# Kernel tuning notes

Measured on AMD Instinct MI355X. Metric: run time of the kernel, lower is better.

Reference implementation:

```python
import jax, jax.numpy as jnp
import numpy as np

EPS = 1e-5  # BatchNorm1d default eps
DIMS = [(784, 1024), (1024, 1024), (1024, 1024), (1024, 10)]


def setup_inputs() -> dict:
    key = jax.random.key(0)
    ks = jax.random.split(key, 25)
    d = {"x": jax.random.normal(ks[0], (32768, 784), jnp.float32)}
    for i, (fi, fo) in enumerate(DIMS):
        j = i + 1
        base = 1 + 6 * i
        d[f"W{j}"] = jax.random.uniform(ks[base], (fo, fi), jnp.float32, -1.0, 1.0)
        d[f"b{j}"] = jnp.full((fo,), 0.01, jnp.float32)
        d[f"gamma{j}"] = jax.random.uniform(ks[base + 1], (fo,), jnp.float32, 0.5, 1.5)
        d[f"beta{j}"] = 0.1 * jax.random.normal(ks[base + 2], (fo,), jnp.float32)
        d[f"mean{j}"] = 0.1 * jax.random.normal(ks[base + 3], (fo,), jnp.float32)
        d[f"var{j}"] = jax.random.uniform(ks[base + 4], (fo,), jnp.float32, 0.5, 1.5)
    return d


def _bn(h, gamma, beta, mean, var):
    # inference-mode BatchNorm1d with running stats
    return gamma * (h - mean) * jax.lax.rsqrt(var + EPS) + beta


def reference(x,
              W1, b1, gamma1, beta1, mean1, var1,
              W2, b2, gamma2, beta2, mean2, var2,
              W3, b3, gamma3, beta3, mean3, var3,
              W4, b4, gamma4, beta4, mean4, var4):
    h = x.reshape(-1, 784)
    # layer 1: Quantizer(1) -> BinarizeLinear -> BN -> Hardtanh
    h = jnp.sign(h)
    h = h @ jnp.sign(W1).T + b1
    h = jnp.clip(_bn(h, gamma1, beta1, mean1, var1), -1.0, 1.0)
    # layer 2
    h = jnp.sign(h)
    h = h @ jnp.sign(W2).T + b2
    h = jnp.clip(_bn(h, gamma2, beta2, mean2, var2), -1.0, 1.0)
    # layer 3
    h = jnp.sign(h)
    h = h @ jnp.sign(W3).T + b3
    h = jnp.clip(_bn(h, gamma3, beta3, mean3, var3), -1.0, 1.0)
    # layer 4: Quantizer -> BinarizeLinear -> BN (no hardtanh)
    h = jnp.sign(h)
    h = h @ jnp.sign(W4).T + b4
    return _bn(h, gamma4, beta4, mean4, var4)
```

## Files before the change

kernel.cpp:

```cpp
#include <hip/hip_runtime.h>
#include <cstdint>
#include <climits>


typedef __attribute__((ext_vector_type(4))) int i32x4_t;

__device__ __forceinline__ void gload_lds16(const void* g, void* l) {
  __builtin_amdgcn_global_load_lds(
      (const __attribute__((address_space(1))) unsigned int*)g,
      (__attribute__((address_space(3))) unsigned int*)l, 16, 0, 0);
}

__device__ __forceinline__ int pack4(const float4 v) {
  int b0 = v.x > 0.f ? 1 : (v.x < 0.f ? -1 : 0);
  int b1 = v.y > 0.f ? 1 : (v.y < 0.f ? -1 : 0);
  int b2 = v.z > 0.f ? 1 : (v.z < 0.f ? -1 : 0);
  int b3 = v.w > 0.f ? 1 : (v.w < 0.f ? -1 : 0);
  return (b0 & 0xff) | ((b1 & 0xff) << 8) | ((b2 & 0xff) << 16) | (b3 << 24);
}


__global__ __launch_bounds__(256) void prep_mega_kernel(
    const float* __restrict__ x, int8_t* __restrict__ A0,
    const float* __restrict__ W1f, const float* __restrict__ W2f,
    const float* __restrict__ W3f, const float* __restrict__ W4f,
    int8_t* __restrict__ Wp1, int8_t* __restrict__ Wp2,
    int8_t* __restrict__ Wp3, int8_t* __restrict__ Wp4,
    const float* b1, const float* g1, const float* be1, const float* m1, const float* v1,
    const float* b2, const float* g2, const float* be2, const float* m2, const float* v2,
    const float* b3, const float* g3, const float* be3, const float* m3, const float* v3,
    const float* b4, const float* g4, const float* be4, const float* m4, const float* v4,
    int* __restrict__ T1, int* __restrict__ T2, int* __restrict__ T3,
    int8_t* __restrict__ S1, int8_t* __restrict__ S2, int8_t* __restrict__ S3,
    float* __restrict__ sc4, float* __restrict__ of4) {
  const int b = blockIdx.x;
  const int t = threadIdx.x;
  if (b < 32768) {
    const int col = t * 4;
    if (col < 784) {
      int packed = pack4(*(const float4*)(x + (size_t)b * 784 + col));
      *(int*)(A0 + (size_t)b * 832 + col) = packed;
    } else if (col < 832) {
      *(int*)(A0 + (size_t)b * 832 + col) = 0;
    }
  } else if (b < 35968) {
    const int b2i = b - 32768;
    const float* Wf; int8_t* Wp; int N, K, n, ost;
    if (b2i < 1024)      { Wf = W1f; Wp = Wp1; N = 1024; K = 784;  n = b2i;        ost = 832;  }
    else if (b2i < 2048) { Wf = W2f; Wp = Wp2; N = 1024; K = 1024; n = b2i - 1024; ost = 1024; }
    else if (b2i < 3072) { Wf = W3f; Wp = Wp3; N = 1024; K = 1024; n = b2i - 2048; ost = 1024; }
    else                 { Wf = W4f; Wp = Wp4; N = 10;   K = 1024; n = b2i - 3072; ost = 1024; }
    const int col = t * 4;
    if (col < ost) {
      int packed = 0;
      if (n < N && col + 3 < K)
        packed = pack4(*(const float4*)(Wf + (size_t)n * K + col));
      *(int*)(Wp + (size_t)n * ost + col) = packed;
    }
  } else {
    const int pb = b - 35968;
    if (pb < 12) {
      const int layer = pb >> 2;
      const int n = (pb & 3) * 256 + t;
      const float *bb, *gg, *be, *me, *va; int* T; int8_t* S;
      if (layer == 0)      { bb = b1; gg = g1; be = be1; me = m1; va = v1; T = T1; S = S1; }
      else if (layer == 1) { bb = b2; gg = g2; be = be2; me = m2; va = v2; T = T2; S = S2; }
      else                 { bb = b3; gg = g3; be = be3; me = m3; va = v3; T = T3; S = S3; }
      double g = (double)gg[n];
      double rs = 1.0 / sqrt((double)va[n] + 1e-5);
      int th; int8_t s;
      if (g > 0.0) {
        double tv = (double)me[n] - (double)bb[n] - (double)be[n] / (g * rs);
        tv = fmin(fmax(tv, -2.0e9), 2.0e9);
        th = (int)floor(tv) + 1; s = 1;
      } else if (g < 0.0) {
        double tv = (double)me[n] - (double)bb[n] - (double)be[n] / (g * rs);
        tv = fmin(fmax(tv, -2.0e9), 2.0e9);
        th = (int)ceil(tv); s = -1;
      } else {
        th = INT_MIN; s = (be[n] > 0.f) ? (int8_t)1 : (int8_t)-1;
      }
      T[n] = th; S[n] = s;
    } else if (t < 10) {
      double rs = 1.0 / sqrt((double)v4[t] + 1e-5);
      double sd = (double)g4[t] * rs;
      sc4[t] = (float)sd;
      of4[t] = (float)(sd * ((double)b4[t] - (double)m4[t]) + (double)be4[t]);
    }
  }
}

__global__ __launch_bounds__(512) void gemm_bnn256_kernel(
    const int8_t* __restrict__ A, const int8_t* __restrict__ W,
    int ldk, int nkt,
    const int* __restrict__ T, const int8_t* __restrict__ S,
    int8_t* __restrict__ Aout) {
  __shared__ i32x4_t smem[4096];
  int8_t* sm = (int8_t*)smem;
  const int tid = threadIdx.x;
  const int lane = tid & 63;
  const int w = tid >> 6;
  const int wm = w >> 2, wn = w & 3;

  const int bid = blockIdx.x;
  const int swz = (bid & 7) * 64 + (bid >> 3);
  const int row0 = (swz >> 2) * 256;
  const int col0 = (swz & 3) * 256;

  const int jj0 = tid, jj1 = tid + 512;
  const int r0 = jj0 >> 2, r1 = jj1 >> 2;
  const int s0 = (jj0 & 3) ^ ((r0 >> 1) & 3);
  const int s1 = (jj1 & 3) ^ ((r1 >> 1) & 3);
  const int8_t* aS0 = A + (size_t)(row0 + r0) * ldk + s0 * 16;
  const int8_t* aS1 = A + (size_t)(row0 + r1) * ldk + s1 * 16;
  const int8_t* bS0 = W + (size_t)(col0 + r0) * ldk + s0 * 16;
  const int8_t* bS1 = W + (size_t)(col0 + r1) * ldk + s1 * 16;
  const int dA0 = jj0 * 16, dA1 = jj1 * 16;
  const int dB0 = 16384 + jj0 * 16, dB1 = 16384 + jj1 * 16;

  int a_off[8], b_off[4];
#pragma unroll
  for (int m = 0; m < 8; ++m) {
    int ra = wm * 128 + m * 16 + (lane & 15);
    a_off[m] = ra * 64 + ((((lane >> 4) ^ (ra >> 1)) & 3) << 4);
  }
#pragma unroll
  for (int n = 0; n < 4; ++n) {
    int rb = wn * 64 + n * 16 + (lane & 15);
    b_off[n] = 16384 + rb * 64 + ((((lane >> 4) ^ (rb >> 1)) & 3) << 4);
  }

  i32x4_t acc[8][4];
#pragma unroll
  for (int m = 0; m < 8; ++m)
#pragma unroll
    for (int n = 0; n < 4; ++n) acc[m][n] = (i32x4_t){0, 0, 0, 0};

  gload_lds16(aS0, sm + dA0);
  gload_lds16(aS1, sm + dA1);
  gload_lds16(bS0, sm + dB0);
  gload_lds16(bS1, sm + dB1);

  for (int kt = 0; kt < nkt; ++kt) {
    const int nxt = kt + 1;
    int8_t* const bufw = sm + ((nxt & 1) << 15);
    const int8_t* const bufr = sm + ((kt & 1) << 15);

    if (nxt < nkt) {
      aS0 += 64; aS1 += 64;
      gload_lds16(aS0, bufw + dA0);
      gload_lds16(aS1, bufw + dA1);
      asm volatile("s_waitcnt vmcnt(2)" ::: "memory");
    } else {
      asm volatile("s_waitcnt vmcnt(0)" ::: "memory");
    }
    asm volatile("s_barrier" ::: "memory");

    i32x4_t bv[4];
#pragma unroll
    for (int i = 0; i < 4; ++i) bv[i] = *(const i32x4_t*)(bufr + b_off[i]);
    {
      i32x4_t av[4];
#pragma unroll
      for (int i = 0; i < 4; ++i) av[i] = *(const i32x4_t*)(bufr + a_off[i]);
      __builtin_amdgcn_s_setprio(1);
#pragma unroll
      for (int m = 0; m < 4; ++m)
#pragma unroll
        for (int n = 0; n < 4; ++n)
          acc[m][n] = __builtin_amdgcn_mfma_i32_16x16x64_i8(av[m], bv[n], acc[m][n], 0, 0, 0);
      __builtin_amdgcn_s_setprio(0);
    }
    asm volatile("s_barrier" ::: "memory");

    if (nxt < nkt) {
      bS0 += 64; bS1 += 64;
      gload_lds16(bS0, bufw + dB0);
      gload_lds16(bS1, bufw + dB1);
    }
    {
      i32x4_t av[4];
#pragma unroll
      for (int i = 0; i < 4; ++i) av[i] = *(const i32x4_t*)(bufr + a_off[4 + i]);
      __builtin_amdgcn_s_setprio(1);
#pragma unroll
      for (int m = 0; m < 4; ++m)
#pragma unroll
        for (int n = 0; n < 4; ++n)
          acc[4 + m][n] = __builtin_amdgcn_mfma_i32_16x16x64_i8(av[m], bv[n], acc[4 + m][n], 0, 0, 0);
      __builtin_amdgcn_s_setprio(0);
    }
    asm volatile("s_barrier" ::: "memory");
  }

#pragma unroll
  for (int n = 0; n < 4; ++n) {
    const int oc = col0 + wn * 64 + n * 16 + (lane & 15);
    const int tn = T[oc];
    const int8_t sn = S[oc];
#pragma unroll
    for (int m = 0; m < 8; ++m) {
      const int orb = row0 + wm * 128 + m * 16 + ((lane >> 4) << 2);
#pragma unroll
      for (int r = 0; r < 4; ++r) {
        int8_t v = (acc[m][n][r] >= tn) ? sn : (int8_t)(-sn);
        Aout[(size_t)(orb + r) * 1024 + oc] = v;
      }
    }
  }
}

__global__ __launch_bounds__(256) void gemm_final_kernel(
    const int8_t* __restrict__ A, const int8_t* __restrict__ W,
    int ldk, int nkt,
    const float* __restrict__ scale, const float* __restrict__ offs,
    float* __restrict__ out) {
  __shared__ i32x4_t smem[2048];
  int8_t* sm = (int8_t*)smem;
  const int tid = threadIdx.x;
  const int lane = tid & 63;
  const int w = tid >> 6;
  const int wrow = w >> 1, wcol = w & 1;
  const int row0 = blockIdx.x * 128;
  const int col0 = 0;

  const int jj0 = tid, jj1 = tid + 256;
  const int r0 = jj0 >> 2, r1 = jj1 >> 2;
  const int s0 = (jj0 & 3) ^ ((r0 >> 1) & 3);
  const int s1 = (jj1 & 3) ^ ((r1 >> 1) & 3);
  const int8_t* aS0 = A + (size_t)(row0 + r0) * ldk + s0 * 16;
  const int8_t* aS1 = A + (size_t)(row0 + r1) * ldk + s1 * 16;
  const int8_t* bS0 = W + (size_t)(col0 + r0) * ldk + s0 * 16;
  const int8_t* bS1 = W + (size_t)(col0 + r1) * ldk + s1 * 16;
  const int dA0 = jj0 * 16, dA1 = jj1 * 16;
  const int dB0 = 8192 + jj0 * 16, dB1 = 8192 + jj1 * 16;

  int a_off[4], b_off[4];
#pragma unroll
  for (int i = 0; i < 4; ++i) {
    int ra = wrow * 64 + i * 16 + (lane & 15);
    a_off[i] = ra * 64 + ((((lane >> 4) ^ (ra >> 1)) & 3) << 4);
    int rb = wcol * 64 + i * 16 + (lane & 15);
    b_off[i] = 8192 + rb * 64 + ((((lane >> 4) ^ (rb >> 1)) & 3) << 4);
  }

  i32x4_t acc[4][4];
#pragma unroll
  for (int m = 0; m < 4; ++m)
#pragma unroll
    for (int n = 0; n < 4; ++n) acc[m][n] = (i32x4_t){0, 0, 0, 0};

  gload_lds16(aS0, sm + dA0);
  gload_lds16(aS1, sm + dA1);
  gload_lds16(bS0, sm + dB0);
  gload_lds16(bS1, sm + dB1);

  for (int kt = 0; kt < nkt - 1; ++kt) {
    aS0 += 64; aS1 += 64; bS0 += 64; bS1 += 64;
    int8_t* smw = sm + (((kt + 1) & 1) << 14);
    gload_lds16(aS0, smw + dA0);
    gload_lds16(aS1, smw + dA1);
    gload_lds16(bS0, smw + dB0);
    gload_lds16(bS1, smw + dB1);
    asm volatile("s_waitcnt vmcnt(4)" ::: "memory");
    asm volatile("s_barrier" ::: "memory");
    const int8_t* smr = sm + ((kt & 1) << 14);
    i32x4_t av[4], bv[4];
#pragma unroll
    for (int i = 0; i < 4; ++i) av[i] = *(const i32x4_t*)(smr + a_off[i]);
#pragma unroll
    for (int i = 0; i < 4; ++i) bv[i] = *(const i32x4_t*)(smr + b_off[i]);
#pragma unroll
    for (int m = 0; m < 4; ++m)
#pragma unroll
      for (int n = 0; n < 4; ++n)
        acc[m][n] = __builtin_amdgcn_mfma_i32_16x16x64_i8(av[m], bv[n], acc[m][n], 0, 0, 0);
    asm volatile("s_barrier" ::: "memory");
  }
  asm volatile("s_waitcnt vmcnt(0)" ::: "memory");
  asm volatile("s_barrier" ::: "memory");
  {
    const int8_t* smr = sm + (((nkt - 1) & 1) << 14);
    i32x4_t av[4], bv[4];
#pragma unroll
    for (int i = 0; i < 4; ++i) av[i] = *(const i32x4_t*)(smr + a_off[i]);
#pragma unroll
    for (int i = 0; i < 4; ++i) bv[i] = *(const i32x4_t*)(smr + b_off[i]);
#pragma unroll
    for (int m = 0; m < 4; ++m)
#pragma unroll
      for (int n = 0; n < 4; ++n)
        acc[m][n] = __builtin_amdgcn_mfma_i32_16x16x64_i8(av[m], bv[n], acc[m][n], 0, 0, 0);
  }

#pragma unroll
  for (int n = 0; n < 4; ++n) {
    const int oc = col0 + wcol * 64 + n * 16 + (lane & 15);
    if (oc < 10) {
      const float sc = scale[oc], of = offs[oc];
#pragma unroll
      for (int m = 0; m < 4; ++m) {
        const int orb = row0 + wrow * 64 + m * 16 + ((lane >> 4) << 2);
#pragma unroll
        for (int r = 0; r < 4; ++r)
          out[(size_t)(orb + r) * 10 + oc] = sc * (float)acc[m][n][r] + of;
      }
    }
  }
}


#define A0_STRIDE 28

__global__ __launch_bounds__(256) void pack_w_kernel(
    const float* __restrict__ W, uint32_t* __restrict__ Wp,
    int nout, int K, int wstride) {
  int idx = blockIdx.x * blockDim.x + threadIdx.x;
  if (idx >= nout * wstride) return;
  int n = idx / wstride;
  int wi = idx - n * wstride;
  const float* wr = W + (size_t)n * K;
  uint32_t word = 0;
  int base = wi * 32;
  for (int i = 0; i < 32; ++i) {
    int c = base + i;
    if (c < K && wr[c] > 0.f) word |= (1u << i);
  }
  Wp[idx] = word;
}

__global__ __launch_bounds__(256) void prep_thr_kernel(
    const float* __restrict__ b, const float* __restrict__ gamma,
    const float* __restrict__ beta, const float* __restrict__ mean,
    const float* __restrict__ var, int K, int N,
    int* __restrict__ thr, uint32_t* __restrict__ flipm) {
  int n = blockIdx.x * blockDim.x + threadIdx.x;
  if (n >= N) return;
  double g = (double)gamma[n];
  double rs = 1.0 / sqrt((double)var[n] + 1e-5);
  int th;
  if (g != 0.0) {
    double t = (double)mean[n] - (double)b[n] - (double)beta[n] / (g * rs);
    double pt = ((double)K - t) * 0.5;
    th = (g > 0.0) ? (int)ceil(pt) : ((int)floor(pt) + 1);
  } else {
    th = (beta[n] > 0.f) ? (K + 2) : -1;
  }
  thr[n] = th;
  if ((n & 31) == 0) {
    uint32_t m = 0;
    for (int i = 0; i < 32 && (n + i) < N; ++i)
      if (gamma[n + i] < 0.f) m |= (1u << i);
    flipm[n >> 5] = m;
  }
}

__global__ __launch_bounds__(64) void prep_out_kernel(
    const float* __restrict__ b, const float* __restrict__ gamma,
    const float* __restrict__ beta, const float* __restrict__ mean,
    const float* __restrict__ var, int N,
    float* __restrict__ s, float* __restrict__ o) {
  int n = threadIdx.x;
  if (n >= N) return;
  double rs = 1.0 / sqrt((double)var[n] + 1e-5);
  double sd = (double)gamma[n] * rs;
  s[n] = (float)sd;
  o[n] = (float)(sd * ((double)b[n] - (double)mean[n]) + (double)beta[n]);
}

__global__ __launch_bounds__(256) void pack_a_kernel(
    const float* __restrict__ x, uint32_t* __restrict__ A0) {
  int gt = blockIdx.x * blockDim.x + threadIdx.x;
  int wv = gt >> 6;
  int lane = gt & 63;
  int row = wv / 13;
  int seg = wv - row * 13;
  int col = (seg << 6) + lane;
  bool pred = (col < 784) && (x[(size_t)row * 784 + col] > 0.f);
  unsigned long long m = __ballot(pred);
  int widx = seg * 2;
  if (lane == 0)
    A0[(size_t)row * A0_STRIDE + widx] = (uint32_t)m;
  else if (lane == 1 && widx + 1 < 25)
    A0[(size_t)row * A0_STRIDE + widx + 1] = (uint32_t)(m >> 32);
}

__device__ __forceinline__ void layer1024(
    uint32_t a[32], const uint32_t* __restrict__ Wp,
    const int* __restrict__ thr, const uint32_t* __restrict__ fm,
    uint32_t* lds, int lane, int w) {
  const int nb = w * 128;
  uint32_t word = 0;
#pragma unroll 2
  for (int ni = 0; ni < 128; ++ni) {
    const int n = nb + ni;
    const uint32_t* __restrict__ wp = Wp + n * 32;
    uint32_t p0 = 0, p1 = 0, p2 = 0, p3 = 0;
#pragma unroll
    for (int k = 0; k < 32; k += 4) {
      p0 += __popc(a[k + 0] ^ wp[k + 0]);
      p1 += __popc(a[k + 1] ^ wp[k + 1]);
      p2 += __popc(a[k + 2] ^ wp[k + 2]);
      p3 += __popc(a[k + 3] ^ wp[k + 3]);
    }
    int p = (int)(p0 + p1 + p2 + p3);
    word |= ((p < thr[n]) ? 1u : 0u) << (ni & 31);
    if ((ni & 31) == 31) {
      lds[lane * 33 + (n >> 5)] = word ^ fm[n >> 5];
      word = 0;
    }
  }
  __syncthreads();
#pragma unroll
  for (int k = 0; k < 32; ++k) a[k] = lds[lane * 33 + k];
  __syncthreads();
}

__global__ __launch_bounds__(512, 4) void fused_kernel(
    const uint32_t* __restrict__ A0,
    const uint32_t* __restrict__ Wp1, const int* __restrict__ thr1, const uint32_t* __restrict__ fm1,
    const uint32_t* __restrict__ Wp2, const int* __restrict__ thr2, const uint32_t* __restrict__ fm2,
    const uint32_t* __restrict__ Wp3, const int* __restrict__ thr3, const uint32_t* __restrict__ fm3,
    const uint32_t* __restrict__ Wp4, const float* __restrict__ s4, const float* __restrict__ o4,
    float* __restrict__ out) {
  __shared__ uint32_t lds[64 * 33];
  const int lane = threadIdx.x & 63;
  const int w = __builtin_amdgcn_readfirstlane((int)(threadIdx.x >> 6));
  const int row = blockIdx.x * 64 + lane;

  uint32_t a[32];
  {
    const uint4* A4 = (const uint4*)(A0 + (size_t)row * A0_STRIDE);
#pragma unroll
    for (int i = 0; i < 7; ++i) {
      uint4 q = A4[i];
      a[4 * i + 0] = q.x; a[4 * i + 1] = q.y; a[4 * i + 2] = q.z; a[4 * i + 3] = q.w;
    }
  }
  {
    const int nb = w * 128;
    uint32_t word = 0;
#pragma unroll 2
    for (int ni = 0; ni < 128; ++ni) {
      const int n = nb + ni;
      const uint32_t* __restrict__ wp = Wp1 + n * A0_STRIDE;
      uint32_t p0 = 0, p1 = 0, p2 = 0, p3 = 0;
#pragma unroll
      for (int k = 0; k < 24; k += 4) {
        p0 += __popc(a[k + 0] ^ wp[k + 0]);
        p1 += __popc(a[k + 1] ^ wp[k + 1]);
        p2 += __popc(a[k + 2] ^ wp[k + 2]);
        p3 += __popc(a[k + 3] ^ wp[k + 3]);
      }
      p0 += __popc(a[24] ^ wp[24]);
      int p = (int)(p0 + p1 + p2 + p3);
      word |= ((p < thr1[n]) ? 1u : 0u) << (ni & 31);
      if ((ni & 31) == 31) {
        lds[lane * 33 + (n >> 5)] = word ^ fm1[n >> 5];
        word = 0;
      }
    }
    __syncthreads();
#pragma unroll
    for (int k = 0; k < 32; ++k) a[k] = lds[lane * 33 + k];
    __syncthreads();
  }
  layer1024(a, Wp2, thr2, fm2, lds, lane, w);
  layer1024(a, Wp3, thr3, fm3, lds, lane, w);
  for (int j = w; j < 10; j += 8) {
    const uint32_t* __restrict__ wp = Wp4 + j * 32;
    uint32_t p0 = 0, p1 = 0, p2 = 0, p3 = 0;
#pragma unroll
    for (int k = 0; k < 32; k += 4) {
      p0 += __popc(a[k + 0] ^ wp[k + 0]);
      p1 += __popc(a[k + 1] ^ wp[k + 1]);
      p2 += __popc(a[k + 2] ^ wp[k + 2]);
      p3 += __popc(a[k + 3] ^ wp[k + 3]);
    }
    float dotf = 1024.f - 2.f * (float)(p0 + p1 + p2 + p3);
    out[(size_t)row * 10 + j] = s4[j] * dotf + o4[j];
  }
}

extern "C" void kernel_launch(void* const* d_in, const int* in_sizes, int n_in,
                              void* d_out, int out_size, void* d_ws, size_t ws_size,
                              hipStream_t stream) {
  const float* x   = (const float*)d_in[0];
  const float* W1  = (const float*)d_in[1];
  const float* b1  = (const float*)d_in[2];
  const float* g1  = (const float*)d_in[3];
  const float* be1 = (const float*)d_in[4];
  const float* m1  = (const float*)d_in[5];
  const float* v1  = (const float*)d_in[6];
  const float* W2  = (const float*)d_in[7];
  const float* b2  = (const float*)d_in[8];
  const float* g2  = (const float*)d_in[9];
  const float* be2 = (const float*)d_in[10];
  const float* m2  = (const float*)d_in[11];
  const float* v2  = (const float*)d_in[12];
  const float* W3  = (const float*)d_in[13];
  const float* b3  = (const float*)d_in[14];
  const float* g3  = (const float*)d_in[15];
  const float* be3 = (const float*)d_in[16];
  const float* m3  = (const float*)d_in[17];
  const float* v3  = (const float*)d_in[18];
  const float* W4  = (const float*)d_in[19];
  const float* b4  = (const float*)d_in[20];
  const float* g4  = (const float*)d_in[21];
  const float* be4 = (const float*)d_in[22];
  const float* m4  = (const float*)d_in[23];
  const float* v4  = (const float*)d_in[24];
  float* outp = (float*)d_out;
  (void)in_sizes; (void)n_in; (void)out_size;

  uint8_t* ws = (uint8_t*)d_ws;
  const size_t NEED = 100ULL << 20;

  if (ws_size >= NEED) {
    size_t off = 0;
    int8_t* A0  = (int8_t*)(ws + off); off += (size_t)32768 * 832;
    int8_t* Bp1 = (int8_t*)(ws + off); off += (size_t)32768 * 1024;
    int8_t* Bp2 = (int8_t*)(ws + off); off += (size_t)32768 * 1024;
    int8_t* Wp1 = (int8_t*)(ws + off); off += (size_t)1024 * 832;
    int8_t* Wp2 = (int8_t*)(ws + off); off += (size_t)1024 * 1024;
    int8_t* Wp3 = (int8_t*)(ws + off); off += (size_t)1024 * 1024;
    int8_t* Wp4 = (int8_t*)(ws + off); off += (size_t)128 * 1024;
    int* T1     = (int*)(ws + off);    off += 4096;
    int* T2     = (int*)(ws + off);    off += 4096;
    int* T3     = (int*)(ws + off);    off += 4096;
    int8_t* S1  = (int8_t*)(ws + off); off += 1024;
    int8_t* S2  = (int8_t*)(ws + off); off += 1024;
    int8_t* S3  = (int8_t*)(ws + off); off += 1024;
    float* sc4  = (float*)(ws + off);  off += 512;
    float* of4  = (float*)(ws + off);  off += 512;

    prep_mega_kernel<<<35981, 256, 0, stream>>>(
        x, A0, W1, W2, W3, W4, Wp1, Wp2, Wp3, Wp4,
        b1, g1, be1, m1, v1, b2, g2, be2, m2, v2,
        b3, g3, be3, m3, v3, b4, g4, be4, m4, v4,
        T1, T2, T3, S1, S2, S3, sc4, of4);

    gemm_bnn256_kernel<<<512, 512, 0, stream>>>(A0, Wp1, 832, 13, T1, S1, Bp1);
    gemm_bnn256_kernel<<<512, 512, 0, stream>>>(Bp1, Wp2, 1024, 16, T2, S2, Bp2);
    gemm_bnn256_kernel<<<512, 512, 0, stream>>>(Bp2, Wp3, 1024, 16, T3, S3, Bp1);
    gemm_final_kernel<<<256, 256, 0, stream>>>(Bp1, Wp4, 1024, 16, sc4, of4, outp);
  } else {
    size_t off = 0;
    uint32_t* A0  = (uint32_t*)(ws + off); off += (size_t)32768 * A0_STRIDE * 4;
    uint32_t* Wp1 = (uint32_t*)(ws + off); off += (size_t)1024 * A0_STRIDE * 4;
    uint32_t* Wp2 = (uint32_t*)(ws + off); off += (size_t)1024 * 32 * 4;
    uint32_t* Wp3 = (uint32_t*)(ws + off); off += (size_t)1024 * 32 * 4;
    uint32_t* Wp4 = (uint32_t*)(ws + off); off += 4096;
    int* thr1     = (int*)(ws + off);      off += 4096;
    int* thr2     = (int*)(ws + off);      off += 4096;
    int* thr3     = (int*)(ws + off);      off += 4096;
    uint32_t* fm1 = (uint32_t*)(ws + off); off += 128;
    uint32_t* fm2 = (uint32_t*)(ws + off); off += 128;
    uint32_t* fm3 = (uint32_t*)(ws + off); off += 128;
    float* s4o    = (float*)(ws + off);    off += 64;
    float* o4o    = (float*)(ws + off);    off += 64;

    pack_w_kernel<<<(1024 * A0_STRIDE + 255) / 256, 256, 0, stream>>>(W1, Wp1, 1024, 784, A0_STRIDE);
    pack_w_kernel<<<(1024 * 32 + 255) / 256, 256, 0, stream>>>(W2, Wp2, 1024, 1024, 32);
    pack_w_kernel<<<(1024 * 32 + 255) / 256, 256, 0, stream>>>(W3, Wp3, 1024, 1024, 32);
    pack_w_kernel<<<(10 * 32 + 255) / 256, 256, 0, stream>>>(W4, Wp4, 10, 1024, 32);
    prep_thr_kernel<<<4, 256, 0, stream>>>(b1, g1, be1, m1, v1, 784, 1024, thr1, fm1);
    prep_thr_kernel<<<4, 256, 0, stream>>>(b2, g2, be2, m2, v2, 1024, 1024, thr2, fm2);
    prep_thr_kernel<<<4, 256, 0, stream>>>(b3, g3, be3, m3, v3, 1024, 1024, thr3, fm3);
    prep_out_kernel<<<1, 64, 0, stream>>>(b4, g4, be4, m4, v4, 10, s4o, o4o);
    pack_a_kernel<<<(32768 * 13) / 4, 256, 0, stream>>>(x, A0);
    fused_kernel<<<512, 512, 0, stream>>>(A0, Wp1, thr1, fm1, Wp2, thr2, fm2,
                                          Wp3, thr3, fm3, Wp4, s4o, o4o, outp);
  }
}
```

Baseline: 328.8 us.

## Switch binary GEMM to 128x256 tiles with 256 threads, two blocks per CU

```diff
diff --git a/kernel.cpp b/kernel.cpp
--- a/kernel.cpp
+++ b/kernel.cpp
@@ -90,44 +90,51 @@
   }
 }
 
-__global__ __launch_bounds__(512) void gemm_bnn256_kernel(
+__global__ __launch_bounds__(256, 2) void gemm_bnn128x256_kernel(
     const int8_t* __restrict__ A, const int8_t* __restrict__ W,
     int ldk, int nkt,
     const int* __restrict__ T, const int8_t* __restrict__ S,
     int8_t* __restrict__ Aout) {
-  __shared__ i32x4_t smem[4096];
+  __shared__ i32x4_t smem[3072];
   int8_t* sm = (int8_t*)smem;
   const int tid = threadIdx.x;
   const int lane = tid & 63;
-  const int w = tid >> 6;
-  const int wm = w >> 2, wn = w & 3;
+  const int wn = tid >> 6;
 
   const int bid = blockIdx.x;
-  const int swz = (bid & 7) * 64 + (bid >> 3);
-  const int row0 = (swz >> 2) * 256;
+  const int swz = (bid & 7) * 128 + (bid >> 3);
+  const int row0 = (swz >> 2) * 128;
   const int col0 = (swz & 3) * 256;
 
-  const int jj0 = tid, jj1 = tid + 512;
-  const int r0 = jj0 >> 2, r1 = jj1 >> 2;
-  const int s0 = (jj0 & 3) ^ ((r0 >> 1) & 3);
-  const int s1 = (jj1 & 3) ^ ((r1 >> 1) & 3);
-  const int8_t* aS0 = A + (size_t)(row0 + r0) * ldk + s0 * 16;
-  const int8_t* aS1 = A + (size_t)(row0 + r1) * ldk + s1 * 16;
-  const int8_t* bS0 = W + (size_t)(col0 + r0) * ldk + s0 * 16;
-  const int8_t* bS1 = W + (size_t)(col0 + r1) * ldk + s1 * 16;
-  const int dA0 = jj0 * 16, dA1 = jj1 * 16;
-  const int dB0 = 16384 + jj0 * 16, dB1 = 16384 + jj1 * 16;
+  const int jA0 = tid, jA1 = tid + 256;
+  const int rA0 = jA0 >> 2, rA1 = jA1 >> 2;
+  const int sA0 = (jA0 & 3) ^ ((rA0 >> 1) & 3);
+  const int sA1 = (jA1 & 3) ^ ((rA1 >> 1) & 3);
+  const int8_t* aS0 = A + (size_t)(row0 + rA0) * ldk + sA0 * 16;
+  const int8_t* aS1 = A + (size_t)(row0 + rA1) * ldk + sA1 * 16;
+  const int dA0 = jA0 * 16, dA1 = jA1 * 16;
+
+  const int8_t* bSrc[4];
+  int dB[4];
+#pragma unroll
+  for (int k = 0; k < 4; ++k) {
+    const int j = tid + 256 * k;
+    const int r = j >> 2;
+    const int s = (j & 3) ^ ((r >> 1) & 3);
+    bSrc[k] = W + (size_t)(col0 + r) * ldk + s * 16;
+    dB[k] = 8192 + j * 16;
+  }
 
   int a_off[8], b_off[4];
 #pragma unroll
   for (int m = 0; m < 8; ++m) {
-    int ra = wm * 128 + m * 16 + (lane & 15);
+    int ra = m * 16 + (lane & 15);
     a_off[m] = ra * 64 + ((((lane >> 4) ^ (ra >> 1)) & 3) << 4);
   }
 #pragma unroll
   for (int n = 0; n < 4; ++n) {
     int rb = wn * 64 + n * 16 + (lane & 15);
-    b_off[n] = 16384 + rb * 64 + ((((lane >> 4) ^ (rb >> 1)) & 3) << 4);
+    b_off[n] = 8192 + rb * 64 + ((((lane >> 4) ^ (rb >> 1)) & 3) << 4);
   }
 
   i32x4_t acc[8][4];
@@ -138,58 +145,40 @@
 
   gload_lds16(aS0, sm + dA0);
   gload_lds16(aS1, sm + dA1);
-  gload_lds16(bS0, sm + dB0);
-  gload_lds16(bS1, sm + dB1);
+#pragma unroll
+  for (int k = 0; k < 4; ++k) gload_lds16(bSrc[k], sm + dB[k]);
 
   for (int kt = 0; kt < nkt; ++kt) {
     const int nxt = kt + 1;
-    int8_t* const bufw = sm + ((nxt & 1) << 15);
-    const int8_t* const bufr = sm + ((kt & 1) << 15);
-
+    const int8_t* const bufr = sm + ((kt & 1) ? 24576 : 0);
     if (nxt < nkt) {
+      int8_t* const bufw = sm + ((nxt & 1) ? 24576 : 0);
       aS0 += 64; aS1 += 64;
       gload_lds16(aS0, bufw + dA0);
       gload_lds16(aS1, bufw + dA1);
-      asm volatile("s_waitcnt vmcnt(2)" ::: "memory");
+#pragma unroll
+      for (int k = 0; k < 4; ++k) {
+        bSrc[k] += 64;
+        gload_lds16(bSrc[k], bufw + dB[k]);
+      }
+      asm volatile("s_waitcnt vmcnt(6)" ::: "memory");
     } else {
       asm volatile("s_waitcnt vmcnt(0)" ::: "memory");
     }
     asm volatile("s_barrier" ::: "memory");
 
-    i32x4_t bv[4];
+    i32x4_t av[8], bv[4];
+#pragma unroll
+    for (int i = 0; i < 8; ++i) av[i] = *(const i32x4_t*)(bufr + a_off[i]);
 #pragma unroll
     for (int i = 0; i < 4; ++i) bv[i] = *(const i32x4_t*)(bufr + b_off[i]);
-    {
-      i32x4_t av[4];
-#pragma unroll
-      for (int i = 0; i < 4; ++i) av[i] = *(const i32x4_t*)(bufr + a_off[i]);
-      __builtin_amdgcn_s_setprio(1);
-#pragma unroll
-      for (int m = 0; m < 4; ++m)
-#pragma unroll
-        for (int n = 0; n < 4; ++n)
-          acc[m][n] = __builtin_amdgcn_mfma_i32_16x16x64_i8(av[m], bv[n], acc[m][n], 0, 0, 0);
-      __builtin_amdgcn_s_setprio(0);
-    }
-    asm volatile("s_barrier" ::: "memory");
-
-    if (nxt < nkt) {
-      bS0 += 64; bS1 += 64;
-      gload_lds16(bS0, bufw + dB0);
-      gload_lds16(bS1, bufw + dB1);
-    }
-    {
-      i32x4_t av[4];
-#pragma unroll
-      for (int i = 0; i < 4; ++i) av[i] = *(const i32x4_t*)(bufr + a_off[4 + i]);
-      __builtin_amdgcn_s_setprio(1);
-#pragma unroll
-      for (int m = 0; m < 4; ++m)
-#pragma unroll
-        for (int n = 0; n < 4; ++n)
-          acc[4 + m][n] = __builtin_amdgcn_mfma_i32_16x16x64_i8(av[m], bv[n], acc[4 + m][n], 0, 0, 0);
-      __builtin_amdgcn_s_setprio(0);
-    }
+    __builtin_amdgcn_s_setprio(1);
+#pragma unroll
+    for (int m = 0; m < 8; ++m)
+#pragma unroll
+      for (int n = 0; n < 4; ++n)
+        acc[m][n] = __builtin_amdgcn_mfma_i32_16x16x64_i8(av[m], bv[n], acc[m][n], 0, 0, 0);
+    __builtin_amdgcn_s_setprio(0);
     asm volatile("s_barrier" ::: "memory");
   }
 
@@ -200,7 +189,7 @@
     const int8_t sn = S[oc];
 #pragma unroll
     for (int m = 0; m < 8; ++m) {
-      const int orb = row0 + wm * 128 + m * 16 + ((lane >> 4) << 2);
+      const int orb = row0 + m * 16 + ((lane >> 4) << 2);
 #pragma unroll
       for (int r = 0; r < 4; ++r) {
         int8_t v = (acc[m][n][r] >= tn) ? sn : (int8_t)(-sn);
@@ -540,9 +529,9 @@
         b3, g3, be3, m3, v3, b4, g4, be4, m4, v4,
         T1, T2, T3, S1, S2, S3, sc4, of4);
 
-    gemm_bnn256_kernel<<<512, 512, 0, stream>>>(A0, Wp1, 832, 13, T1, S1, Bp1);
-    gemm_bnn256_kernel<<<512, 512, 0, stream>>>(Bp1, Wp2, 1024, 16, T2, S2, Bp2);
-    gemm_bnn256_kernel<<<512, 512, 0, stream>>>(Bp2, Wp3, 1024, 16, T3, S3, Bp1);
+    gemm_bnn128x256_kernel<<<1024, 256, 0, stream>>>(A0, Wp1, 832, 13, T1, S1, Bp1);
+    gemm_bnn128x256_kernel<<<1024, 256, 0, stream>>>(Bp1, Wp2, 1024, 16, T2, S2, Bp2);
+    gemm_bnn128x256_kernel<<<1024, 256, 0, stream>>>(Bp2, Wp3, 1024, 16, T3, S3, Bp1);
     gemm_final_kernel<<<256, 256, 0, stream>>>(Bp1, Wp4, 1024, 16, sc4, of4, outp);
   } else {
     size_t off = 0;
```

New measurement: 318.3 us. 1.03x faster.

## Triple-buffer LDS prefetch in int8 BNN GEMM and restructure MFMA phases

Applied to the files above, without the earlier changes.

```diff
diff --git a/kernel.cpp b/kernel.cpp
--- a/kernel.cpp
+++ b/kernel.cpp
@@ -90,12 +90,12 @@
   }
 }
 
-__global__ __launch_bounds__(512) void gemm_bnn256_kernel(
+__global__ __launch_bounds__(512, 2) void gemm_bnn256p_kernel(
     const int8_t* __restrict__ A, const int8_t* __restrict__ W,
     int ldk, int nkt,
     const int* __restrict__ T, const int8_t* __restrict__ S,
     int8_t* __restrict__ Aout) {
-  __shared__ i32x4_t smem[4096];
+  __shared__ i32x4_t smem[6144];
   int8_t* sm = (int8_t*)smem;
   const int tid = threadIdx.x;
   const int lane = tid & 63;
@@ -107,16 +107,17 @@
   const int row0 = (swz >> 2) * 256;
   const int col0 = (swz & 3) * 256;
 
-  const int jj0 = tid, jj1 = tid + 512;
-  const int r0 = jj0 >> 2, r1 = jj1 >> 2;
-  const int s0 = (jj0 & 3) ^ ((r0 >> 1) & 3);
-  const int s1 = (jj1 & 3) ^ ((r1 >> 1) & 3);
-  const int8_t* aS0 = A + (size_t)(row0 + r0) * ldk + s0 * 16;
-  const int8_t* aS1 = A + (size_t)(row0 + r1) * ldk + s1 * 16;
-  const int8_t* bS0 = W + (size_t)(col0 + r0) * ldk + s0 * 16;
-  const int8_t* bS1 = W + (size_t)(col0 + r1) * ldk + s1 * 16;
-  const int dA0 = jj0 * 16, dA1 = jj1 * 16;
-  const int dB0 = 16384 + jj0 * 16, dB1 = 16384 + jj1 * 16;
+  const int8_t* gsrc[4];
+  int gdst[4];
+#pragma unroll
+  for (int h = 0; h < 4; ++h) {
+    const int j = (h & 1) * 512 + tid;
+    const int r = j >> 2;
+    const int s = (j & 3) ^ ((r >> 1) & 3);
+    gsrc[h] = ((h >= 2) ? (W + (size_t)(col0 + r) * ldk)
+                        : (A + (size_t)(row0 + r) * ldk)) + s * 16;
+    gdst[h] = ((h >= 2) ? 16384 : 0) + j * 16;
+  }
 
   int a_off[8], b_off[4];
 #pragma unroll
@@ -136,61 +137,64 @@
 #pragma unroll
     for (int n = 0; n < 4; ++n) acc[m][n] = (i32x4_t){0, 0, 0, 0};
 
-  gload_lds16(aS0, sm + dA0);
-  gload_lds16(aS1, sm + dA1);
-  gload_lds16(bS0, sm + dB0);
-  gload_lds16(bS1, sm + dB1);
-
+#pragma unroll
+  for (int h = 0; h < 4; ++h) { gload_lds16(gsrc[h], sm + gdst[h]); gsrc[h] += 64; }
+#pragma unroll
+  for (int h = 0; h < 4; ++h) { gload_lds16(gsrc[h], sm + 32768 + gdst[h]); gsrc[h] += 64; }
+
+  int bufr = 0;
   for (int kt = 0; kt < nkt; ++kt) {
-    const int nxt = kt + 1;
-    int8_t* const bufw = sm + ((nxt & 1) << 15);
-    const int8_t* const bufr = sm + ((kt & 1) << 15);
-
-    if (nxt < nkt) {
-      aS0 += 64; aS1 += 64;
-      gload_lds16(aS0, bufw + dA0);
-      gload_lds16(aS1, bufw + dA1);
-      asm volatile("s_waitcnt vmcnt(2)" ::: "memory");
+    if (kt + 2 < nkt) {
+      int bufw = bufr + 65536; if (bufw >= 98304) bufw -= 98304;
+#pragma unroll
+      for (int h = 0; h < 4; ++h) { gload_lds16(gsrc[h], sm + bufw + gdst[h]); gsrc[h] += 64; }
+      asm volatile("s_waitcnt vmcnt(8)" ::: "memory");
+    } else if (kt + 1 < nkt) {
+      asm volatile("s_waitcnt vmcnt(4)" ::: "memory");
     } else {
       asm volatile("s_waitcnt vmcnt(0)" ::: "memory");
     }
     asm volatile("s_barrier" ::: "memory");
 
-    i32x4_t bv[4];
-#pragma unroll
-    for (int i = 0; i < 4; ++i) bv[i] = *(const i32x4_t*)(bufr + b_off[i]);
-    {
-      i32x4_t av[4];
-#pragma unroll
-      for (int i = 0; i < 4; ++i) av[i] = *(const i32x4_t*)(bufr + a_off[i]);
-      __builtin_amdgcn_s_setprio(1);
-#pragma unroll
-      for (int m = 0; m < 4; ++m)
-#pragma unroll
-        for (int n = 0; n < 4; ++n)
-          acc[m][n] = __builtin_amdgcn_mfma_i32_16x16x64_i8(av[m], bv[n], acc[m][n], 0, 0, 0);
-      __builtin_amdgcn_s_setprio(0);
-    }
+    const int8_t* const bb = sm + bufr;
+    i32x4_t av[8], bv[4];
+
+#pragma unroll
+    for (int i = 0; i < 4; ++i) av[i] = *(const i32x4_t*)(bb + a_off[i]);
+    bv[0] = *(const i32x4_t*)(bb + b_off[0]);
+    bv[1] = *(const i32x4_t*)(bb + b_off[1]);
     asm volatile("s_barrier" ::: "memory");
-
-    if (nxt < nkt) {
-      bS0 += 64; bS1 += 64;
-      gload_lds16(bS0, bufw + dB0);
-      gload_lds16(bS1, bufw + dB1);
-    }
-    {
-      i32x4_t av[4];
-#pragma unroll
-      for (int i = 0; i < 4; ++i) av[i] = *(const i32x4_t*)(bufr + a_off[4 + i]);
-      __builtin_amdgcn_s_setprio(1);
-#pragma unroll
-      for (int m = 0; m < 4; ++m)
-#pragma unroll
-        for (int n = 0; n < 4; ++n)
-          acc[4 + m][n] = __builtin_amdgcn_mfma_i32_16x16x64_i8(av[m], bv[n], acc[4 + m][n], 0, 0, 0);
-      __builtin_amdgcn_s_setprio(0);
-    }
+    __builtin_amdgcn_s_setprio(1);
+#pragma unroll
+    for (int m = 0; m < 4; ++m)
+#pragma unroll
+      for (int n = 0; n < 2; ++n)
+        acc[m][n] = __builtin_amdgcn_mfma_i32_16x16x64_i8(av[m], bv[n], acc[m][n], 0, 0, 0);
+    __builtin_amdgcn_s_setprio(0);
+
+#pragma unroll
+    for (int i = 0; i < 4; ++i) av[4 + i] = *(const i32x4_t*)(bb + a_off[4 + i]);
     asm volatile("s_barrier" ::: "memory");
+    __builtin_amdgcn_s_setprio(1);
+#pragma unroll
+    for (int m = 0; m < 4; ++m)
+#pragma unroll
+      for (int n = 0; n < 2; ++n)
+        acc[4 + m][n] = __builtin_amdgcn_mfma_i32_16x16x64_i8(av[4 + m], bv[n], acc[4 + m][n], 0, 0, 0);
+    __builtin_amdgcn_s_setprio(0);
+
+    bv[2] = *(const i32x4_t*)(bb + b_off[2]);
+    bv[3] = *(const i32x4_t*)(bb + b_off[3]);
+    asm volatile("s_barrier" ::: "memory");
+    __builtin_amdgcn_s_setprio(1);
+#pragma unroll
+    for (int m = 0; m < 8; ++m)
+#pragma unroll
+      for (int n = 2; n < 4; ++n)
+        acc[m][n] = __builtin_amdgcn_mfma_i32_16x16x64_i8(av[m], bv[n], acc[m][n], 0, 0, 0);
+    __builtin_amdgcn_s_setprio(0);
+
+    bufr += 32768; if (bufr >= 98304) bufr = 0;
   }
 
 #pragma unroll
@@ -540,9 +544,9 @@
         b3, g3, be3, m3, v3, b4, g4, be4, m4, v4,
         T1, T2, T3, S1, S2, S3, sc4, of4);
 
-    gemm_bnn256_kernel<<<512, 512, 0, stream>>>(A0, Wp1, 832, 13, T1, S1, Bp1);
-    gemm_bnn256_kernel<<<512, 512, 0, stream>>>(Bp1, Wp2, 1024, 16, T2, S2, Bp2);
-    gemm_bnn256_kernel<<<512, 512, 0, stream>>>(Bp2, Wp3, 1024, 16, T3, S3, Bp1);
+    gemm_bnn256p_kernel<<<512, 512, 0, stream>>>(A0, Wp1, 832, 13, T1, S1, Bp1);
+    gemm_bnn256p_kernel<<<512, 512, 0, stream>>>(Bp1, Wp2, 1024, 16, T2, S2, Bp2);
+    gemm_bnn256p_kernel<<<512, 512, 0, stream>>>(Bp2, Wp3, 1024, 16, T3, S3, Bp1);
     gemm_final_kernel<<<256, 256, 0, stream>>>(Bp1, Wp4, 1024, 16, sc4, of4, outp);
   } else {
     size_t off = 0;
```

Measured after the change: 322.4 us. About the same (-2.0%).
